# Kernel tuning notes

Hardware: AMD Instinct MI355X
Metric: run time of the kernel (lower is better)

The kernel has to match this reference:

```python
import jax, jax.numpy as jnp
import numpy as np

N_HEADS = 16
D_MODEL = 1024
HEAD_DIM = D_MODEL // N_HEADS
B, S = 2, 2048


def setup_inputs() -> dict:
    key = jax.random.key(0)
    ks = jax.random.split(key, 10)
    scale = 1.0 / np.sqrt(D_MODEL)
    inp = {
        "query_tokens": jax.random.normal(ks[0], (B, S, D_MODEL), dtype=jnp.float32),
        "key_or_value_tokens": jax.random.normal(ks[1], (B, S, D_MODEL), dtype=jnp.float32),
        "mask": jnp.ones((B, S, S), dtype=jnp.int32),
        "Wq": jax.random.normal(ks[2], (D_MODEL, D_MODEL), dtype=jnp.float32) * scale,
        "bq": jnp.zeros((D_MODEL,), dtype=jnp.float32),
        "Wk": jax.random.normal(ks[3], (D_MODEL, D_MODEL), dtype=jnp.float32) * scale,
        "bk": jnp.zeros((D_MODEL,), dtype=jnp.float32),
        "Wv": jax.random.normal(ks[4], (D_MODEL, D_MODEL), dtype=jnp.float32) * scale,
        "bv": jnp.zeros((D_MODEL,), dtype=jnp.float32),
        "Wo": jax.random.normal(ks[5], (D_MODEL, D_MODEL), dtype=jnp.float32) * scale,
        "bo": jnp.zeros((D_MODEL,), dtype=jnp.float32),
    }
    return inp


def reference(query_tokens, key_or_value_tokens, mask, Wq, bq, Wk, bk, Wv, bv, Wo, bo):
    b, s, d = query_tokens.shape
    h, dh = N_HEADS, HEAD_DIM

    def proj(x, W, bias):
        # torch Linear: x @ W.T + b ; then split heads -> (b, h, s, dh)
        y = jnp.einsum("bsd,ed->bse", x, W) + bias
        return y.reshape(b, -1, h, dh).transpose(0, 2, 1, 3)

    q = proj(query_tokens, Wq, bq)
    k = proj(key_or_value_tokens, Wk, bk)
    v = proj(key_or_value_tokens, Wv, bv)

    scores = jnp.einsum("bhqd,bhkd->bhqk", q, k) / jnp.sqrt(jnp.float32(dh))
    # mask: (b, Sq, Sk) -> (b, 1, Sq, Sk); zeros get large negative fill
    scores = jnp.where(mask[:, None, :, :] == 0, jnp.float32(-1e9), scores)
    attn = jax.nn.softmax(scores, axis=-1)
    out = jnp.einsum("bhqk,bhkd->bhqd", attn, v)
    out = out.transpose(0, 2, 1, 3).reshape(b, s, d)
    return jnp.einsum("bsd,ed->bse", out, Wo) + bo
```

## Files before the change

kernel.cpp:

```cpp
#include <hip/hip_runtime.h>
#include <hip/hip_bf16.h>

typedef __bf16 bf16_8  __attribute__((ext_vector_type(8)));
typedef __bf16 bf16_4  __attribute__((ext_vector_type(4)));
typedef float  f32_4   __attribute__((ext_vector_type(4)));

#define NH 16
#define DHD 64
#define BB 2
#define SS 2048
#define DD 1024

__device__ __forceinline__ void gload16(const __bf16* g, __bf16* l) {
    __builtin_amdgcn_global_load_lds(
        (const __attribute__((address_space(1))) void*)g,
        (__attribute__((address_space(3))) void*)l, 16, 0, 0);
}

__global__ __launch_bounds__(256) void conv_all(
    const float* __restrict__ s0, const float* __restrict__ s1,
    const float* __restrict__ s2, const float* __restrict__ s3,
    const float* __restrict__ s4, const float* __restrict__ s5,
    __bf16* __restrict__ d0, __bf16* __restrict__ d1, __bf16* __restrict__ d2,
    __bf16* __restrict__ d3, __bf16* __restrict__ d4, __bf16* __restrict__ d5) {
    const int y = blockIdx.y;
    if (y >= 2 && blockIdx.x >= 1024) return;
    const float* s = (y == 0) ? s0 : (y == 1) ? s1 : (y == 2) ? s2
                   : (y == 3) ? s3 : (y == 4) ? s4 : s5;
    __bf16* d      = (y == 0) ? d0 : (y == 1) ? d1 : (y == 2) ? d2
                   : (y == 3) ? d3 : (y == 4) ? d4 : d5;
    const int i = (blockIdx.x * 256 + threadIdx.x) * 4;
    f32_4 v = *(const f32_4*)&s[i];
    bf16_4 o; o[0] = (__bf16)v[0]; o[1] = (__bf16)v[1];
    o[2] = (__bf16)v[2]; o[3] = (__bf16)v[3];
    *(bf16_4*)&d[i] = o;
}

__global__ __launch_bounds__(256) void mask_flags_k(const int* __restrict__ mask,
                                                    int* __restrict__ flags) {
    const int id = blockIdx.x;
    const int b = id >> 10, qt = (id >> 5) & 31, kt = id & 31;
    const int t = threadIdx.x;
    const int row = t >> 2, seg = t & 3;
    const int* p = mask + ((size_t)b * SS + qt * 64 + row) * SS + kt * 64 + seg * 16;
    int any0 = 0;
#pragma unroll
    for (int i = 0; i < 4; ++i) {
        int4 v = *(const int4*)&p[i * 4];
        any0 |= (v.x == 0) | (v.y == 0) | (v.z == 0) | (v.w == 0);
    }
    unsigned long long bal = __ballot(any0);
    __shared__ int sf[4];
    if ((t & 63) == 0) sf[t >> 6] = (bal != 0ULL);
    __syncthreads();
    if (t == 0) flags[id] = sf[0] | sf[1] | sf[2] | sf[3];
}

template <int LAYOUT>
__device__ __forceinline__ void gemm_body(const __bf16* __restrict__ A,
                                          const __bf16* __restrict__ W,
                                          const float* __restrict__ bias,
                                          __bf16* __restrict__ out,
                                          __bf16* ldsA0, __bf16* ldsB0,
                                          __bf16* ldsA1, __bf16* ldsB1) {
    const int tid  = threadIdx.x;
    const int lane = tid & 63;
    const int w    = tid >> 6;
    const int quad = lane >> 4;
    const int l15  = lane & 15;
    const int wm   = (w >> 1) * 64;
    const int wn   = (w & 1) * 64;
    const int m0   = blockIdx.x * 128;
    const int n0   = blockIdx.y * 128;

    f32_4 acc[4][4] = {};

#define QSTAGE(KT, LA, LB)                                                     \
    do {                                                                       \
        _Pragma("unroll") for (int cc = 0; cc < 2; ++cc) {                     \
            const int c   = tid + cc * 256;                                    \
            const int row = c >> 2;                                            \
            const int cp  = c & 3;                                             \
            gload16(&A[(size_t)(m0 + row) * 1024 + (KT) + cp * 8],             \
                    &(LA)[c * 8]);                                             \
            gload16(&W[(size_t)(n0 + row) * 1024 + (KT) + cp * 8],             \
                    &(LB)[c * 8]);                                             \
        }                                                                      \
    } while (0)

    QSTAGE(0, ldsA0, ldsB0);
    __syncthreads();

    for (int kt = 0; kt < 1024; kt += 32) {
        const int sel = (kt >> 5) & 1;
        const __bf16* la = sel ? ldsA1 : ldsA0;
        const __bf16* lb = sel ? ldsB1 : ldsB0;
        __bf16* na       = sel ? ldsA0 : ldsA1;
        __bf16* nb       = sel ? ldsB0 : ldsB1;
        if (kt + 32 < 1024) QSTAGE(kt + 32, na, nb);

        bf16_8 af[4], bfr[4];
#pragma unroll
        for (int i = 0; i < 4; ++i)
            af[i] = *(const bf16_8*)&la[(wm + i * 16 + l15) * 32 + quad * 8];
#pragma unroll
        for (int j = 0; j < 4; ++j)
            bfr[j] = *(const bf16_8*)&lb[(wn + j * 16 + l15) * 32 + quad * 8];
#pragma unroll
        for (int i = 0; i < 4; ++i)
#pragma unroll
            for (int j = 0; j < 4; ++j)
                acc[i][j] = __builtin_amdgcn_mfma_f32_16x16x32_bf16(
                    af[i], bfr[j], acc[i][j], 0, 0, 0);

        __syncthreads();
    }
#undef QSTAGE

#pragma unroll
    for (int i = 0; i < 4; ++i) {
#pragma unroll
        for (int j = 0; j < 4; ++j) {
            const int col = n0 + wn + j * 16 + l15;
            const float bv = bias[col];
            if (LAYOUT == 2) {
                const int row0 = m0 + wm + i * 16 + quad * 4;
                bf16_4 pk;
#pragma unroll
                for (int r = 0; r < 4; ++r) pk[r] = (__bf16)(acc[i][j][r] + bv);
                const int bb = row0 >> 11, s0 = row0 & 2047;
                const int h = col >> 6, dh = col & 63;
                *(bf16_4*)&out[(((size_t)bb * NH + h) * DHD + dh) * SS + s0] = pk;
            } else {
#pragma unroll
                for (int r = 0; r < 4; ++r) {
                    const int row = m0 + wm + i * 16 + quad * 4 + r;
                    out[(((size_t)(row >> 11) * NH + (col >> 6)) * SS +
                         (row & 2047)) * DHD + (col & 63)] =
                        (__bf16)(acc[i][j][r] + bv);
                }
            }
        }
    }
}

__global__ __launch_bounds__(256) void gemm_qkv(
    const __bf16* __restrict__ Xq, const __bf16* __restrict__ Xkv,
    const __bf16* __restrict__ Wq, const float* __restrict__ bq,
    const __bf16* __restrict__ Wk, const float* __restrict__ bk,
    const __bf16* __restrict__ Wv, const float* __restrict__ bv,
    __bf16* __restrict__ Qo, __bf16* __restrict__ Ko, __bf16* __restrict__ VTo) {
    __shared__ __align__(16) __bf16 ldsA0[128 * 32];
    __shared__ __align__(16) __bf16 ldsB0[128 * 32];
    __shared__ __align__(16) __bf16 ldsA1[128 * 32];
    __shared__ __align__(16) __bf16 ldsB1[128 * 32];
    const int z = blockIdx.z;
    const __bf16* A    = (z == 0) ? Xq : Xkv;
    const __bf16* W    = (z == 0) ? Wq : (z == 1 ? Wk : Wv);
    const float* bias  = (z == 0) ? bq : (z == 1 ? bk : bv);
    if (z == 2)
        gemm_body<2>(A, W, bias, VTo, ldsA0, ldsB0, ldsA1, ldsB1);
    else
        gemm_body<0>(A, W, bias, (z == 0) ? Qo : Ko, ldsA0, ldsB0, ldsA1, ldsB1);
}

__global__ __launch_bounds__(256) void gemm_final(
    const __bf16* __restrict__ A, const __bf16* __restrict__ W,
    const float* __restrict__ bias, float* __restrict__ out) {
    __shared__ __align__(16) __bf16 ldsA0[128 * 32];
    __shared__ __align__(16) __bf16 ldsB0[64 * 32];
    __shared__ __align__(16) __bf16 ldsA1[128 * 32];
    __shared__ __align__(16) __bf16 ldsB1[64 * 32];
    const int tid  = threadIdx.x;
    const int lane = tid & 63;
    const int w    = tid >> 6;
    const int quad = lane >> 4;
    const int l15  = lane & 15;
    const int wm   = w * 32;
    const int m0   = blockIdx.x * 128;
    const int n0   = blockIdx.y * 64;

    f32_4 acc[2][4] = {};

#define FSTAGE(KT, LA, LB)                                                     \
    do {                                                                       \
        _Pragma("unroll") for (int cc = 0; cc < 2; ++cc) {                     \
            const int c   = tid + cc * 256;                                    \
            const int row = c >> 2;                                            \
            const int cp  = c & 3;                                             \
            gload16(&A[(size_t)(m0 + row) * 1024 + (KT) + cp * 8],             \
                    &(LA)[c * 8]);                                             \
        }                                                                      \
        {                                                                      \
            const int c   = tid;                                               \
            const int row = c >> 2;                                            \
            const int cp  = c & 3;                                             \
            gload16(&W[(size_t)(n0 + row) * 1024 + (KT) + cp * 8],             \
                    &(LB)[c * 8]);                                             \
        }                                                                      \
    } while (0)

    FSTAGE(0, ldsA0, ldsB0);
    __syncthreads();

    for (int kt = 0; kt < 1024; kt += 32) {
        const int sel = (kt >> 5) & 1;
        const __bf16* la = sel ? ldsA1 : ldsA0;
        const __bf16* lb = sel ? ldsB1 : ldsB0;
        __bf16* na       = sel ? ldsA0 : ldsA1;
        __bf16* nb       = sel ? ldsB0 : ldsB1;
        if (kt + 32 < 1024) FSTAGE(kt + 32, na, nb);

        bf16_8 af[2], bfr[4];
#pragma unroll
        for (int i = 0; i < 2; ++i)
            af[i] = *(const bf16_8*)&la[(wm + i * 16 + l15) * 32 + quad * 8];
#pragma unroll
        for (int j = 0; j < 4; ++j)
            bfr[j] = *(const bf16_8*)&lb[(j * 16 + l15) * 32 + quad * 8];
#pragma unroll
        for (int i = 0; i < 2; ++i)
#pragma unroll
            for (int j = 0; j < 4; ++j)
                acc[i][j] = __builtin_amdgcn_mfma_f32_16x16x32_bf16(
                    af[i], bfr[j], acc[i][j], 0, 0, 0);

        __syncthreads();
    }
#undef FSTAGE

#pragma unroll
    for (int i = 0; i < 2; ++i)
#pragma unroll
        for (int j = 0; j < 4; ++j) {
            const int col = n0 + j * 16 + l15;
            const float bv = bias[col];
#pragma unroll
            for (int r = 0; r < 4; ++r) {
                const int row = m0 + wm + i * 16 + quad * 4 + r;
                out[(size_t)row * 1024 + col] = acc[i][j][r] + bv;
            }
        }
}

__global__ __launch_bounds__(256, 2) void flash_attn(
    const __bf16* __restrict__ Q, const __bf16* __restrict__ K,
    const __bf16* __restrict__ VT, const int* __restrict__ mask,
    const int* __restrict__ flags, __bf16* __restrict__ O) {
    __shared__ __align__(16) __bf16 ldsK0[64 * 64];
    __shared__ __align__(16) __bf16 ldsK1[64 * 64];
    __shared__ __align__(16) __bf16 ldsV0[64 * 64];
    __shared__ __align__(16) __bf16 ldsV1[64 * 64];
    __shared__ __align__(16) __bf16 ldsP0[128 * 72];
    __shared__ __align__(16) __bf16 ldsP1[128 * 72];

    const int tid  = threadIdx.x;
    const int lane = tid & 63;
    const int w    = tid >> 6;
    const int quad = lane >> 4;
    const int l15  = lane & 15;
    const int q0   = blockIdx.x * 128;
    const int bh   = blockIdx.y;
    const int b    = bh >> 4;

    const __bf16* Qb  = Q + (size_t)bh * SS * DHD;
    const __bf16* Kb  = K + (size_t)bh * SS * DHD;
    const __bf16* VTb = VT + (size_t)bh * DHD * SS;
    const int*    mb  = mask + (size_t)b * SS * SS;
    const int*    flb = flags + (size_t)b * 1024 + blockIdx.x * 64;

    bf16_8 qa[2][2];
#pragma unroll
    for (int mt = 0; mt < 2; ++mt)
#pragma unroll
        for (int ks = 0; ks < 2; ++ks) {
            bf16_8 t = *(const bf16_8*)&Qb[(size_t)(q0 + w * 32 + mt * 16 + l15) * DHD +
                                           ks * 32 + quad * 8];
#pragma unroll
            for (int e = 0; e < 8; ++e)
                qa[mt][ks][e] = (__bf16)((float)t[e] * 0.18033688011112042f);
        }

    bf16_8 ones;
#pragma unroll
    for (int e = 0; e < 8; ++e) ones[e] = (__bf16)1.0f;

    f32_4 of[2][4] = {};
    f32_4 lsum[2] = {};

    const int c0 = tid, c1 = tid + 256;
    const int r_0 = c0 >> 3, r_1 = c1 >> 3;
    const int s_0 = (c0 & 7) ^ (r_0 & 7);
    const int s_1 = (c1 & 7) ^ (r_1 & 7);

#define STAGE_K(K0_, DST)                                                      \
    do {                                                                       \
        gload16(&Kb[(size_t)((K0_) + r_0) * DHD + s_0 * 8], &(DST)[c0 * 8]);   \
        gload16(&Kb[(size_t)((K0_) + r_1) * DHD + s_1 * 8], &(DST)[c1 * 8]);   \
    } while (0)
#define STAGE_V(K0_, DST)                                                      \
    do {                                                                       \
        gload16(&VTb[(size_t)r_0 * SS + (K0_) + s_0 * 8], &(DST)[c0 * 8]);     \
        gload16(&VTb[(size_t)r_1 * SS + (K0_) + s_1 * 8], &(DST)[c1 * 8]);     \
    } while (0)

    const int xq = l15 & 7;

#define QKT(KSRC, SA)                                                          \
    do {                                                                       \
        _Pragma("unroll") for (int ks = 0; ks < 2; ++ks) {                     \
            bf16_8 kb[4];                                                      \
            _Pragma("unroll") for (int j = 0; j < 4; ++j)                      \
                kb[j] = *(const bf16_8*)&(KSRC)[(j * 16 + l15) * 64 +          \
                                                (((ks * 4 + quad) ^ xq) * 8)]; \
            _Pragma("unroll") for (int mt = 0; mt < 2; ++mt)                   \
                _Pragma("unroll") for (int j = 0; j < 4; ++j)                  \
                    SA[mt][j] = __builtin_amdgcn_mfma_f32_16x16x32_bf16(       \
                        kb[j], qa[mt][ks], SA[mt][j], 0, 0, 0);                \
        }                                                                      \
    } while (0)

#define MASKF(TN, SA)                                                          \
    do {                                                                       \
        if ((flb[TN] | flb[32 + (TN)]) != 0) {                                 \
            _Pragma("unroll") for (int mt = 0; mt < 2; ++mt)                   \
                _Pragma("unroll") for (int j = 0; j < 4; ++j)                  \
                    _Pragma("unroll") for (int r = 0; r < 4; ++r) {            \
                        const int qg = q0 + w * 32 + mt * 16 + l15;            \
                        const int kg = (TN) * 64 + j * 16 + quad * 4 + r;      \
                        if (mb[(size_t)qg * SS + kg] == 0) SA[mt][j][r] = -1e9f; \
                    }                                                          \
        }                                                                      \
    } while (0)

#define EXPW(SA, PDST)                                                         \
    do {                                                                       \
        _Pragma("unroll") for (int mt = 0; mt < 2; ++mt)                       \
            _Pragma("unroll") for (int j = 0; j < 4; ++j) {                    \
                bf16_4 pk;                                                     \
                _Pragma("unroll") for (int r = 0; r < 4; ++r)                  \
                    pk[r] = (__bf16)__builtin_amdgcn_exp2f(SA[mt][j][r]);      \
                *(bf16_4*)&(PDST)[(w * 32 + mt * 16 + l15) * 72 + j * 16 +     \
                                  quad * 4] = pk;                              \
            }                                                                  \
    } while (0)

#define PV(VSRC, PSRC)                                                         \
    do {                                                                       \
        _Pragma("unroll") for (int ks2 = 0; ks2 < 2; ++ks2) {                  \
            bf16_8 pa[2], vb[4];                                               \
            _Pragma("unroll") for (int mt = 0; mt < 2; ++mt)                   \
                pa[mt] = *(const bf16_8*)&(PSRC)[(w * 32 + mt * 16 + l15) * 72 \
                                                 + ks2 * 32 + quad * 8];       \
            _Pragma("unroll") for (int jo = 0; jo < 4; ++jo)                   \
                vb[jo] = *(const bf16_8*)&(VSRC)[(jo * 16 + l15) * 64 +        \
                                                 (((ks2 * 4 + quad) ^ xq) * 8)]; \
            __builtin_amdgcn_s_setprio(1);                                     \
            _Pragma("unroll") for (int mt = 0; mt < 2; ++mt) {                 \
                _Pragma("unroll") for (int jo = 0; jo < 4; ++jo)               \
                    of[mt][jo] = __builtin_amdgcn_mfma_f32_16x16x32_bf16(      \
                        pa[mt], vb[jo], of[mt][jo], 0, 0, 0);                  \
                lsum[mt] = __builtin_amdgcn_mfma_f32_16x16x32_bf16(            \
                    pa[mt], ones, lsum[mt], 0, 0, 0);                          \
            }                                                                  \
            __builtin_amdgcn_s_setprio(0);                                     \
        }                                                                      \
    } while (0)

    STAGE_K(0, ldsK0);
    STAGE_V(0, ldsV0);
    __syncthreads();
    STAGE_K(64, ldsK1);
    STAGE_V(64, ldsV1);
    {
        f32_4 sa[2][4] = {};
        QKT(ldsK0, sa);
        MASKF(0, sa);
        EXPW(sa, ldsP0);
    }
    __syncthreads();

    for (int t = 0; t < 31; ++t) {
        const int sel = t & 1;
        __bf16* kst       = sel ? ldsK1 : ldsK0;
        const __bf16* kn  = sel ? ldsK0 : ldsK1;
        const __bf16* vc  = sel ? ldsV1 : ldsV0;
        const __bf16* pc  = sel ? ldsP1 : ldsP0;
        __bf16* pn        = sel ? ldsP0 : ldsP1;
        __bf16* vst       = sel ? ldsV1 : ldsV0;

        if (t < 30) STAGE_K((t + 2) * 64, kst);

        f32_4 sa[2][4] = {};
        QKT(kn, sa);
        MASKF(t + 1, sa);
        PV(vc, pc);
        EXPW(sa, pn);

        __syncthreads();
        if (t < 30) STAGE_V((t + 2) * 64, vst);
    }

    PV(ldsV1, ldsP1);

    const int hcol = (bh & 15) * 64;
#pragma unroll
    for (int mt = 0; mt < 2; ++mt)
#pragma unroll
        for (int r = 0; r < 4; ++r) {
            const float inv = 1.0f / fmaxf(lsum[mt][r], 1e-37f);
            const int qg = q0 + w * 32 + mt * 16 + quad * 4 + r;
#pragma unroll
            for (int jo = 0; jo < 4; ++jo)
                O[((size_t)b * SS + qg) * DD + hcol + jo * 16 + l15] =
                    (__bf16)(of[mt][jo][r] * inv);
        }
#undef STAGE_K
#undef STAGE_V
#undef QKT
#undef MASKF
#undef EXPW
#undef PV
}


extern "C" void kernel_launch(void* const* d_in, const int* in_sizes, int n_in,
                              void* d_out, int out_size, void* d_ws, size_t ws_size,
                              hipStream_t stream) {
    const float* xq   = (const float*)d_in[0];
    const float* xkv  = (const float*)d_in[1];
    const int*   mask = (const int*)d_in[2];
    const float* Wq   = (const float*)d_in[3];
    const float* bq   = (const float*)d_in[4];
    const float* Wk   = (const float*)d_in[5];
    const float* bk   = (const float*)d_in[6];
    const float* Wv   = (const float*)d_in[7];
    const float* bv   = (const float*)d_in[8];
    const float* Wo   = (const float*)d_in[9];
    const float* bo   = (const float*)d_in[10];

    __bf16* ws = (__bf16*)d_ws;
    const size_t big = (size_t)BB * SS * DD;
    const size_t wsz = (size_t)DD * DD;
    __bf16* Qw   = ws;
    __bf16* Kw   = Qw + big;
    __bf16* VTw  = Kw + big;
    __bf16* Aw   = VTw + big;
    __bf16* Xqb  = Aw + big;
    __bf16* Xkvb = Xqb + big;
    __bf16* Wqb  = Xkvb + big;
    __bf16* Wkb  = Wqb + wsz;
    __bf16* Wvb  = Wkb + wsz;
    __bf16* Wob  = Wvb + wsz;
    int* flags   = (int*)(Wob + wsz);

    conv_all<<<dim3(4096, 6), dim3(256), 0, stream>>>(xq, xkv, Wq, Wk, Wv, Wo,
                                                      Xqb, Xkvb, Wqb, Wkb, Wvb, Wob);
    mask_flags_k<<<dim3(2048), dim3(256), 0, stream>>>(mask, flags);
    gemm_qkv<<<dim3(32, 8, 3), dim3(256), 0, stream>>>(Xqb, Xkvb, Wqb, bq, Wkb, bk,
                                                       Wvb, bv, Qw, Kw, VTw);
    flash_attn<<<dim3(SS / 128, BB * NH), dim3(256), 0, stream>>>(Qw, Kw, VTw, mask,
                                                                  flags, Aw);
    gemm_final<<<dim3(32, 16), dim3(256), 0, stream>>>(Aw, Wob, bo, (float*)d_out);
}
```

Before: 235.2 us.

## Triple-buffer GEMM LDS staging with explicit vmcnt waits

Converts the QKV and output-projection GEMMs from double-buffered to triple-buffered LDS staging. Tiles are prefetched two K-steps ahead, and the full __syncthreads is replaced by partial s_waitcnt vmcnt plus s_barrier, so one stage of global loads stays in flight across the barrier. The intent is to hide global-load latency better. The cost is 50% more LDS per block, which can lower occupancy, and hand-counted vmcnt values that must match the number of issued loads.

```diff
diff --git a/kernel.cpp b/kernel.cpp
--- a/kernel.cpp
+++ b/kernel.cpp
@@ -62,7 +62,8 @@
                                           const float* __restrict__ bias,
                                           __bf16* __restrict__ out,
                                           __bf16* ldsA0, __bf16* ldsB0,
-                                          __bf16* ldsA1, __bf16* ldsB1) {
+                                          __bf16* ldsA1, __bf16* ldsB1,
+                                          __bf16* ldsA2, __bf16* ldsB2) {
     const int tid  = threadIdx.x;
     const int lane = tid & 63;
     const int w    = tid >> 6;
@@ -88,24 +89,26 @@
         }                                                                      \
     } while (0)
 
-    QSTAGE(0, ldsA0, ldsB0);
-    __syncthreads();
+    __bf16 *cA = ldsA0, *cB = ldsB0;
+    __bf16 *nA = ldsA1, *nB = ldsB1;
+    __bf16 *tA = ldsA2, *tB = ldsB2;
+
+    QSTAGE(0, cA, cB);
+    QSTAGE(32, nA, nB);
+    asm volatile("s_waitcnt vmcnt(4)" ::: "memory");
+    __builtin_amdgcn_s_barrier();
 
     for (int kt = 0; kt < 1024; kt += 32) {
-        const int sel = (kt >> 5) & 1;
-        const __bf16* la = sel ? ldsA1 : ldsA0;
-        const __bf16* lb = sel ? ldsB1 : ldsB0;
-        __bf16* na       = sel ? ldsA0 : ldsA1;
-        __bf16* nb       = sel ? ldsB0 : ldsB1;
-        if (kt + 32 < 1024) QSTAGE(kt + 32, na, nb);
+        const bool morestage = (kt + 64 < 1024);
+        if (morestage) QSTAGE(kt + 64, tA, tB);
 
         bf16_8 af[4], bfr[4];
 #pragma unroll
         for (int i = 0; i < 4; ++i)
-            af[i] = *(const bf16_8*)&la[(wm + i * 16 + l15) * 32 + quad * 8];
+            af[i] = *(const bf16_8*)&cA[(wm + i * 16 + l15) * 32 + quad * 8];
 #pragma unroll
         for (int j = 0; j < 4; ++j)
-            bfr[j] = *(const bf16_8*)&lb[(wn + j * 16 + l15) * 32 + quad * 8];
+            bfr[j] = *(const bf16_8*)&cB[(wn + j * 16 + l15) * 32 + quad * 8];
 #pragma unroll
         for (int i = 0; i < 4; ++i)
 #pragma unroll
@@ -113,7 +116,15 @@
                 acc[i][j] = __builtin_amdgcn_mfma_f32_16x16x32_bf16(
                     af[i], bfr[j], acc[i][j], 0, 0, 0);
 
-        __syncthreads();
+        if (kt + 32 < 1024) {
+            if (morestage)
+                asm volatile("s_waitcnt vmcnt(4) lgkmcnt(0)" ::: "memory");
+            else
+                asm volatile("s_waitcnt vmcnt(0) lgkmcnt(0)" ::: "memory");
+            __builtin_amdgcn_s_barrier();
+        }
+        __bf16* sA = cA; cA = nA; nA = tA; tA = sA;
+        __bf16* sB = cB; cB = nB; nB = tB; tB = sB;
     }
 #undef QSTAGE
 
@@ -154,14 +165,17 @@
     __shared__ __align__(16) __bf16 ldsB0[128 * 32];
     __shared__ __align__(16) __bf16 ldsA1[128 * 32];
     __shared__ __align__(16) __bf16 ldsB1[128 * 32];
+    __shared__ __align__(16) __bf16 ldsA2[128 * 32];
+    __shared__ __align__(16) __bf16 ldsB2[128 * 32];
     const int z = blockIdx.z;
     const __bf16* A    = (z == 0) ? Xq : Xkv;
     const __bf16* W    = (z == 0) ? Wq : (z == 1 ? Wk : Wv);
     const float* bias  = (z == 0) ? bq : (z == 1 ? bk : bv);
     if (z == 2)
-        gemm_body<2>(A, W, bias, VTo, ldsA0, ldsB0, ldsA1, ldsB1);
+        gemm_body<2>(A, W, bias, VTo, ldsA0, ldsB0, ldsA1, ldsB1, ldsA2, ldsB2);
     else
-        gemm_body<0>(A, W, bias, (z == 0) ? Qo : Ko, ldsA0, ldsB0, ldsA1, ldsB1);
+        gemm_body<0>(A, W, bias, (z == 0) ? Qo : Ko, ldsA0, ldsB0, ldsA1, ldsB1,
+                     ldsA2, ldsB2);
 }
 
 __global__ __launch_bounds__(256) void gemm_final(
@@ -171,6 +185,8 @@
     __shared__ __align__(16) __bf16 ldsB0[64 * 32];
     __shared__ __align__(16) __bf16 ldsA1[128 * 32];
     __shared__ __align__(16) __bf16 ldsB1[64 * 32];
+    __shared__ __align__(16) __bf16 ldsA2[128 * 32];
+    __shared__ __align__(16) __bf16 ldsB2[64 * 32];
     const int tid  = threadIdx.x;
     const int lane = tid & 63;
     const int w    = tid >> 6;
@@ -200,24 +216,26 @@
         }                                                                      \
     } while (0)
 
-    FSTAGE(0, ldsA0, ldsB0);
-    __syncthreads();
+    __bf16 *cA = ldsA0, *cB = ldsB0;
+    __bf16 *nA = ldsA1, *nB = ldsB1;
+    __bf16 *tA = ldsA2, *tB = ldsB2;
+
+    FSTAGE(0, cA, cB);
+    FSTAGE(32, nA, nB);
+    asm volatile("s_waitcnt vmcnt(3)" ::: "memory");
+    __builtin_amdgcn_s_barrier();
 
     for (int kt = 0; kt < 1024; kt += 32) {
-        const int sel = (kt >> 5) & 1;
-        const __bf16* la = sel ? ldsA1 : ldsA0;
-        const __bf16* lb = sel ? ldsB1 : ldsB0;
-        __bf16* na       = sel ? ldsA0 : ldsA1;
-        __bf16* nb       = sel ? ldsB0 : ldsB1;
-        if (kt + 32 < 1024) FSTAGE(kt + 32, na, nb);
+        const bool morestage = (kt + 64 < 1024);
+        if (morestage) FSTAGE(kt + 64, tA, tB);
 
         bf16_8 af[2], bfr[4];
 #pragma unroll
         for (int i = 0; i < 2; ++i)
-            af[i] = *(const bf16_8*)&la[(wm + i * 16 + l15) * 32 + quad * 8];
+            af[i] = *(const bf16_8*)&cA[(wm + i * 16 + l15) * 32 + quad * 8];
 #pragma unroll
         for (int j = 0; j < 4; ++j)
-            bfr[j] = *(const bf16_8*)&lb[(j * 16 + l15) * 32 + quad * 8];
+            bfr[j] = *(const bf16_8*)&cB[(j * 16 + l15) * 32 + quad * 8];
 #pragma unroll
         for (int i = 0; i < 2; ++i)
 #pragma unroll
@@ -225,7 +243,15 @@
                 acc[i][j] = __builtin_amdgcn_mfma_f32_16x16x32_bf16(
                     af[i], bfr[j], acc[i][j], 0, 0, 0);
 
-        __syncthreads();
+        if (kt + 32 < 1024) {
+            if (morestage)
+                asm volatile("s_waitcnt vmcnt(3) lgkmcnt(0)" ::: "memory");
+            else
+                asm volatile("s_waitcnt vmcnt(0) lgkmcnt(0)" ::: "memory");
+            __builtin_amdgcn_s_barrier();
+        }
+        __bf16* sA = cA; cA = nA; nA = tA; tA = sA;
+        __bf16* sB = cB; cB = nB; nB = tB; tB = sB;
     }
 #undef FSTAGE
 
```

Result: slower. 249.0 us (+5.9%).
